# Performance work log

Measured on AMD Instinct MI355X. Metric: run time of the kernel, lower is better.

The kernel has to match this reference:

```python
import jax, jax.numpy as jnp
import numpy as np

NUM_HEADS = 12
EPS = 1e-5


def setup_inputs() -> dict:
    key = jax.random.key(0)
    k0, k1, k2 = jax.random.split(key, 3)
    B, C, D = 2, 768, 14  # batch, hidden_size, img_size//16
    x = jax.random.normal(k0, (B, C, D, D, D), dtype=jnp.float32)
    norm_w = jnp.ones((C,), dtype=jnp.float32)
    norm_b = jnp.zeros((C,), dtype=jnp.float32)
    qkv_w = jax.random.normal(k1, (3 * C, C), dtype=jnp.float32) * 0.02
    out_w = jax.random.normal(k2, (C, C), dtype=jnp.float32) * 0.02
    out_b = jnp.zeros((C,), dtype=jnp.float32)
    return {"x": x, "norm_w": norm_w, "norm_b": norm_b,
            "qkv_w": qkv_w, "out_w": out_w, "out_b": out_b}


def reference(x, norm_w, norm_b, qkv_w, out_w, out_b):
    B, C, D, H, W = x.shape
    nh = NUM_HEADS
    dh = C // nh
    scale = dh ** -0.5

    # b c d h w -> b (d h w) c
    t = jnp.transpose(x, (0, 2, 3, 4, 1)).reshape(B, D * H * W, C)
    N = t.shape[1]

    # LayerNorm over channel dim
    mu = jnp.mean(t, axis=-1, keepdims=True)
    var = jnp.mean(jnp.square(t - mu), axis=-1, keepdims=True)
    tn = (t - mu) / jnp.sqrt(var + EPS) * norm_w + norm_b

    # qkv projection (no bias), split as (3, heads, dim_head)
    qkv = tn @ qkv_w.T                       # [B, N, 3C]
    qkv = qkv.reshape(B, N, 3, nh, dh)
    qkv = jnp.transpose(qkv, (2, 0, 3, 1, 4))  # [3, B, nh, N, dh]
    q, k, v = qkv[0], qkv[1], qkv[2]

    att = jax.nn.softmax(jnp.einsum('blxn,blyn->blxy', q, k) * scale, axis=-1)
    out = jnp.einsum('blxy,blyn->blxn', att, v)  # [B, nh, N, dh]

    out = jnp.transpose(out, (0, 2, 1, 3)).reshape(B, N, C)
    out = out @ out_w.T + out_b

    out = out.reshape(B, D, H, W, C)
    out = jnp.transpose(out, (0, 4, 1, 2, 3))  # b d h w c -> b c d h w
    return out + x
```

## Files before the change

kernel.cpp:

```cpp
#include <hip/hip_runtime.h>

typedef unsigned short u16;
typedef unsigned int u32;

#define SPA 2744
#define CH  768
#define NH  12
#define DH  64
#define BB  2
#define TC  2304
#define MTOT (BB*SPA)
#define LNB 343
#define CVTB 2304

typedef __bf16 bf16x8_t __attribute__((ext_vector_type(8)));
typedef __bf16 bf16x4_t __attribute__((ext_vector_type(4)));
typedef short  s16x4    __attribute__((ext_vector_type(4)));
typedef float  f32x4_t  __attribute__((ext_vector_type(4)));

static __device__ __forceinline__ u16 f2bf(float f) {
    union { float f; u32 u; } v; v.f = f;
    u32 u = v.u;
    u += 0x7fffu + ((u >> 16) & 1u);
    return (u16)(u >> 16);
}

static __device__ __forceinline__ void gld16(const u16* g, u16* l) {
    __builtin_amdgcn_global_load_lds(
        (const __attribute__((address_space(1))) u32*)(size_t)g,
        (__attribute__((address_space(3))) u32*)(u32)(size_t)l, 16, 0, 0);
}

__global__ __launch_bounds__(256) void cvtln_kernel(const float* __restrict__ qkv_w,
                                                    u16* __restrict__ qkvw_bf, int n4a,
                                                    const float* __restrict__ out_w,
                                                    u16* __restrict__ outw_bf,
                                                    const float* __restrict__ x,
                                                    const float* __restrict__ w,
                                                    const float* __restrict__ bta,
                                                    u16* __restrict__ tn) {
    int tid = threadIdx.x;
    if (blockIdx.x >= LNB) {
        int i = (blockIdx.x - LNB) * 256 + tid;
        const float* src; u16* dst; int idx;
        if (i < n4a) { src = qkv_w; dst = qkvw_bf; idx = i; }
        else { src = out_w; dst = outw_bf; idx = i - n4a; }
        float4 f = ((const float4*)src)[idx];
        uint2 o;
        o.x = (u32)f2bf(f.x) | ((u32)f2bf(f.y) << 16);
        o.y = (u32)f2bf(f.z) | ((u32)f2bf(f.w) << 16);
        ((uint2*)dst)[idx] = o;
        return;
    }
    int bid = blockIdx.x;
    __shared__ f32x4_t redS[4][4];
    __shared__ f32x4_t redQ[4][4];
    __shared__ u16 T[64][22];
    int grp = tid & 3, chl = tid >> 2;
    int wvi = tid >> 6, lane = tid & 63;
    int tok0 = bid * 16 + grp * 4;
    int b = tok0 / SPA, n = tok0 - b * SPA;
    const float* base = x + (size_t)b * CH * SPA + n;

    f32x4_t s4 = {0.f, 0.f, 0.f, 0.f}, q4 = {0.f, 0.f, 0.f, 0.f};
    for (int c0 = 0; c0 < CH; c0 += 64) {
        float4 v = *(const float4*)(base + (size_t)(c0 + chl) * SPA);
        s4[0] += v.x; s4[1] += v.y; s4[2] += v.z; s4[3] += v.w;
        q4[0] += v.x * v.x; q4[1] += v.y * v.y; q4[2] += v.z * v.z; q4[3] += v.w * v.w;
    }
#pragma unroll
    for (int m = 4; m <= 32; m <<= 1)
#pragma unroll
        for (int e = 0; e < 4; e++) {
            s4[e] += __shfl_xor(s4[e], m);
            q4[e] += __shfl_xor(q4[e], m);
        }
    if (lane < 4) { redS[wvi][lane] = s4; redQ[wvi][lane] = q4; }
    __syncthreads();
    f32x4_t st = redS[0][grp], qt = redQ[0][grp];
#pragma unroll
    for (int wv2 = 1; wv2 < 4; wv2++) {
        f32x4_t a = redS[wv2][grp], c = redQ[wv2][grp];
#pragma unroll
        for (int e = 0; e < 4; e++) { st[e] += a[e]; qt[e] += c[e]; }
    }
    f32x4_t mean4, rstd4;
#pragma unroll
    for (int e = 0; e < 4; e++) {
        mean4[e] = st[e] * (1.0f / CH);
        rstd4[e] = rsqrtf(qt[e] * (1.0f / CH) - mean4[e] * mean4[e] + 1e-5f);
    }

    int tokl = tid >> 4, qq = tid & 15;
    int g2 = bid * 16 + tokl;
    for (int c0 = 0; c0 < CH; c0 += 64) {
        __syncthreads();
        {
            int cc = c0 + chl;
            float4 v = *(const float4*)(base + (size_t)cc * SPA);
            float ws = w[cc], bs = bta[cc];
            union { u16 h4[4]; uint2 u; } pk;
            pk.h4[0] = f2bf((v.x - mean4[0]) * rstd4[0] * ws + bs);
            pk.h4[1] = f2bf((v.y - mean4[1]) * rstd4[1] * ws + bs);
            pk.h4[2] = f2bf((v.z - mean4[2]) * rstd4[2] * ws + bs);
            pk.h4[3] = f2bf((v.w - mean4[3]) * rstd4[3] * ws + bs);
            *(uint2*)(&T[chl][grp * 4]) = pk.u;
        }
        __syncthreads();
        union { u16 h[4]; uint2 u; } pk;
#pragma unroll
        for (int e = 0; e < 4; e++) pk.h[e] = T[qq * 4 + e][tokl];
        *(uint2*)(tn + (size_t)g2 * CH + c0 + qq * 4) = pk.u;
    }
}

__global__ __launch_bounds__(256, 3) void gemm_qkv(const u16* __restrict__ A,
                                                   const u16* __restrict__ Bw,
                                                   u16* __restrict__ out0,
                                                   u16* __restrict__ out1,
                                                   u16* __restrict__ out2) {
    const int M = MTOT, K = CH;
    __shared__ __align__(16) u16 As[128 * 32];
    __shared__ __align__(16) u16 Bs[128 * 32];
    int tid = threadIdx.x;
    int m0 = blockIdx.y * 128;
    int n0 = blockIdx.x * 128;
    int wv = tid >> 6, lane = tid & 63;
    int wm = (wv >> 1) * 64, wn = (wv & 1) * 64;
    int quad = lane >> 4, l16 = lane & 15;

    f32x4_t zero = {0.f, 0.f, 0.f, 0.f};
    f32x4_t acc[4][4];
#pragma unroll
    for (int i = 0; i < 4; i++)
#pragma unroll
        for (int j = 0; j < 4; j++) acc[i][j] = zero;

    int rl = lane >> 2, pos = lane & 3;
    int sw = (l16 >> 1) & 3;
    for (int k0 = 0; k0 < K; k0 += 32) {
        __syncthreads();
#pragma unroll
        for (int p = 0; p < 2; p++) {
            int rbase = p * 64 + wv * 16;
            int row = rbase + rl;
            int gch = pos ^ ((row >> 1) & 3);
            int gm = m0 + row; if (gm >= M) gm = M - 1;
            gld16(A + (size_t)gm * K + k0 + gch * 8, As + rbase * 32);
            gld16(Bw + (size_t)(n0 + row) * K + k0 + gch * 8, Bs + rbase * 32);
        }
        __syncthreads();
        bf16x8_t af[4], bfr[4];
#pragma unroll
        for (int i = 0; i < 4; i++)
            af[i] = *(const bf16x8_t*)(As + (wm + i * 16 + l16) * 32 + ((quad ^ sw) * 8));
#pragma unroll
        for (int j = 0; j < 4; j++)
            bfr[j] = *(const bf16x8_t*)(Bs + (wn + j * 16 + l16) * 32 + ((quad ^ sw) * 8));
#pragma unroll
        for (int i = 0; i < 4; i++)
#pragma unroll
            for (int j = 0; j < 4; j++)
                acc[i][j] = __builtin_amdgcn_mfma_f32_16x16x32_bf16(af[i], bfr[j], acc[i][j], 0, 0, 0);
    }

    int which = n0 / CH;
    int rb = n0 - which * CH;
    u16* base = (which == 0) ? out0 : ((which == 1) ? out1 : out2);
    float qs = (which == 0) ? 0.18033688011112042f : 1.0f;
#pragma unroll
    for (int i = 0; i < 4; i++)
#pragma unroll
        for (int r = 0; r < 4; r++) {
            int gm = m0 + wm + i * 16 + quad * 4 + r;
            if (gm < M) {
                int b = gm / SPA, n = gm - b * SPA;
#pragma unroll
                for (int j = 0; j < 4; j++) {
                    int rem = rb + wn + j * 16 + l16;
                    int h = rem >> 6, d = rem & 63;
                    base[((size_t)(b * NH + h) * SPA + n) * DH + d] = f2bf(acc[i][j][r] * qs);
                }
            }
        }
}

__global__ __launch_bounds__(256, 4) void gemm_out(const u16* __restrict__ A,
                                                   const u16* __restrict__ Bw,
                                                   const float* __restrict__ xres,
                                                   const float* __restrict__ ob,
                                                   float* __restrict__ fout) {
    const int M = MTOT, K = CH;
    __shared__ __align__(16) u16 As[128 * 32];
    __shared__ __align__(16) u16 Bs[64 * 32];
    int tid = threadIdx.x;
    int m0 = blockIdx.y * 128;
    int n0 = blockIdx.x * 64;
    int wv = tid >> 6, lane = tid & 63;
    int wm = (wv >> 1) * 64, wn = (wv & 1) * 32;
    int quad = lane >> 4, l16 = lane & 15;

    f32x4_t zero = {0.f, 0.f, 0.f, 0.f};
    f32x4_t acc[4][2];
#pragma unroll
    for (int i = 0; i < 4; i++)
#pragma unroll
        for (int j = 0; j < 2; j++) acc[i][j] = zero;

    int rl = lane >> 2, pos = lane & 3;
    int sw = (l16 >> 1) & 3;
    for (int k0 = 0; k0 < K; k0 += 32) {
        __syncthreads();
#pragma unroll
        for (int p = 0; p < 2; p++) {
            int rbase = p * 64 + wv * 16;
            int row = rbase + rl;
            int gch = pos ^ ((row >> 1) & 3);
            int gm = m0 + row; if (gm >= M) gm = M - 1;
            gld16(A + (size_t)gm * K + k0 + gch * 8, As + rbase * 32);
        }
        {
            int row = wv * 16 + rl;
            int gch = pos ^ ((row >> 1) & 3);
            gld16(Bw + (size_t)(n0 + row) * K + k0 + gch * 8, Bs + (wv * 16) * 32);
        }
        __syncthreads();
        bf16x8_t af[4], bfr[2];
#pragma unroll
        for (int i = 0; i < 4; i++)
            af[i] = *(const bf16x8_t*)(As + (wm + i * 16 + l16) * 32 + ((quad ^ sw) * 8));
#pragma unroll
        for (int j = 0; j < 2; j++)
            bfr[j] = *(const bf16x8_t*)(Bs + (wn + j * 16 + l16) * 32 + ((quad ^ sw) * 8));
#pragma unroll
        for (int i = 0; i < 4; i++)
#pragma unroll
            for (int j = 0; j < 2; j++)
                acc[i][j] = __builtin_amdgcn_mfma_f32_16x16x32_bf16(af[i], bfr[j], acc[i][j], 0, 0, 0);
    }

#pragma unroll
    for (int i = 0; i < 4; i++) {
        int gm0 = m0 + wm + i * 16 + quad * 4;
        if (gm0 < M) {
            int b = gm0 / SPA;
            int n = gm0 - b * SPA;
#pragma unroll
            for (int j = 0; j < 2; j++) {
                int gn = n0 + wn + j * 16 + l16;
                size_t xo = ((size_t)(b * CH + gn)) * SPA + n;
                float4 xv = *(const float4*)(xres + xo);
                float bias = ob[gn];
                float4 rr;
                rr.x = xv.x + bias + acc[i][j][0];
                rr.y = xv.y + bias + acc[i][j][1];
                rr.z = xv.z + bias + acc[i][j][2];
                rr.w = xv.w + bias + acc[i][j][3];
                *(float4*)(fout + xo) = rr;
            }
        }
    }
}

__global__ __launch_bounds__(256) void vtrans_kernel(const u16* __restrict__ v,
                                                     u16* __restrict__ vt) {
    __shared__ __align__(16) u16 T[64 * 72];
    int bh = blockIdx.y;
    int n0 = blockIdx.x * 64;
    int tid = threadIdx.x;
#pragma unroll
    for (int h = 0; h < 2; h++) {
        int chunk = tid + h * 256;
        int r = chunk >> 3, cs = chunk & 7;
        int n = n0 + r;
        int4 val = make_int4(0, 0, 0, 0);
        if (n < SPA) val = *(const int4*)(v + ((size_t)bh * SPA + n) * DH + cs * 8);
        *(int4*)(T + r * 72 + cs * 8) = val;
    }
    __syncthreads();
#pragma unroll
    for (int h = 0; h < 2; h++) {
        int chunk = tid + h * 256;
        int d = chunk >> 3, cs = chunk & 7;
        int nb = n0 + cs * 8;
        if (nb < SPA) {
            union { u16 s[8]; int4 v4; } tmp;
#pragma unroll
            for (int e = 0; e < 8; e++) tmp.s[e] = T[(cs * 8 + e) * 72 + d];
            *(int4*)(vt + ((size_t)bh * DH + d) * SPA + nb) = tmp.v4;
        }
    }
}

__global__ __launch_bounds__(256, 3) void attn_kernel(const u16* __restrict__ q,
                                                      const u16* __restrict__ k,
                                                      const u16* __restrict__ vt,
                                                      u16* __restrict__ out) {
    __shared__ __align__(16) u16 Kbuf[2][96 * 64];
    __shared__ __align__(16) u16 Vbuf[2][64 * 108];
    int g = blockIdx.x;
    int xcd = g & 7, slot = g >> 3;
    int bh = xcd * 3 + slot % 3;
    int qg = slot / 3;
    int b = bh / NH, h = bh - b * NH;
    int tid = threadIdx.x;
    int wv = tid >> 6, lane = tid & 63;
    int quad = lane >> 4, l16 = lane & 15;
    int qhalf = wv & 1, khalf = wv >> 1;
    int koff = khalf * 48;
    int q0w = qg * 64 + qhalf * 32;

    const u16* qgp = q + (size_t)bh * SPA * DH;
    const u16* kg = k + (size_t)bh * SPA * DH;
    const u16* vg = vt + (size_t)bh * DH * SPA;

    bf16x8_t bq[2][2];
    int qglob[2];
#pragma unroll
    for (int qf = 0; qf < 2; qf++) {
        int qq = q0w + qf * 16 + l16;
        qglob[qf] = qq;
        int qld = (qq < SPA) ? qq : (SPA - 1);
#pragma unroll
        for (int ks = 0; ks < 2; ks++)
            bq[qf][ks] = *(const bf16x8_t*)(qgp + (size_t)qld * DH + ks * 32 + quad * 8);
    }

    f32x4_t zero = {0.f, 0.f, 0.f, 0.f};
    f32x4_t o[2][4];
#pragma unroll
    for (int qf = 0; qf < 2; qf++)
#pragma unroll
        for (int i = 0; i < 4; i++) o[qf][i] = zero;
    f32x4_t lacc[2];
    lacc[0] = zero; lacc[1] = zero;
    s16x4 ones;
    ones[0] = ones[1] = ones[2] = ones[3] = (short)0x3F80;

    int rl8 = lane >> 3, pos8 = lane & 7;
    int sw8 = l16 & 7;
    int vd = tid >> 2, vc = (tid & 3) * 24;

#pragma unroll
    for (int p = 0; p < 3; p++) {
        int rbase = p * 32 + wv * 8;
        int row = rbase + rl8;
        int gch = pos8 ^ (row & 7);
        gld16(kg + (size_t)row * DH + gch * 8, Kbuf[0] + rbase * 64);
    }
#pragma unroll
    for (int s2 = 0; s2 < 3; s2++)
        *(int4*)(Vbuf[0] + vd * 108 + vc + s2 * 8) =
            *(const int4*)(vg + (size_t)vd * SPA + vc + s2 * 8);

    for (int si = 0; si < 29; si++) {
        __syncthreads();
        int cur = si & 1, nxt = cur ^ 1;
        int kv0 = si * 96;
        bool hn = (si < 28);
        int4 vp0, vp1, vp2;
        if (hn) {
            int kb = kv0 + 96;
#pragma unroll
            for (int p = 0; p < 3; p++) {
                int rbase = p * 32 + wv * 8;
                int row = rbase + rl8;
                int gch = pos8 ^ (row & 7);
                int kr = kb + row; if (kr >= SPA) kr = SPA - 1;
                gld16(kg + (size_t)kr * DH + gch * 8, Kbuf[nxt] + rbase * 64);
            }
            int c0 = kb + vc;
            int a0 = c0;      if (a0 > SPA - 8) a0 = SPA - 8;
            int a1 = c0 + 8;  if (a1 > SPA - 8) a1 = SPA - 8;
            int a2 = c0 + 16; if (a2 > SPA - 8) a2 = SPA - 8;
            vp0 = *(const int4*)(vg + (size_t)vd * SPA + a0);
            vp1 = *(const int4*)(vg + (size_t)vd * SPA + a1);
            vp2 = *(const int4*)(vg + (size_t)vd * SPA + a2);
        }

        s16x4 bp[2][3];
#pragma unroll
        for (int i = 0; i < 3; i++) {
            const u16* krow = Kbuf[cur] + (koff + i * 16 + l16) * 64;
            bf16x8_t ak0 = *(const bf16x8_t*)(krow + ((quad ^ sw8) * 8));
            bf16x8_t ak1 = *(const bf16x8_t*)(krow + (((4 + quad) ^ sw8) * 8));
            f32x4_t s0 = __builtin_amdgcn_mfma_f32_16x16x32_bf16(ak0, bq[0][0], zero, 0, 0, 0);
            s0 = __builtin_amdgcn_mfma_f32_16x16x32_bf16(ak1, bq[0][1], s0, 0, 0, 0);
            f32x4_t s1 = __builtin_amdgcn_mfma_f32_16x16x32_bf16(ak0, bq[1][0], zero, 0, 0, 0);
            s1 = __builtin_amdgcn_mfma_f32_16x16x32_bf16(ak1, bq[1][1], s1, 0, 0, 0);
            bf16x4_t p0, p1;
            if (si != 28) {
#pragma unroll
                for (int r = 0; r < 4; r++) {
                    p0[r] = (__bf16)__builtin_amdgcn_exp2f(s0[r]);
                    p1[r] = (__bf16)__builtin_amdgcn_exp2f(s1[r]);
                }
            } else {
#pragma unroll
                for (int r = 0; r < 4; r++) {
                    float e0 = __builtin_amdgcn_exp2f(s0[r]);
                    float e1 = __builtin_amdgcn_exp2f(s1[r]);
                    bool bad = (kv0 + koff + i * 16 + quad * 4 + r) >= SPA;
                    p0[r] = (__bf16)(bad ? 0.f : e0);
                    p1[r] = (__bf16)(bad ? 0.f : e1);
                }
            }
            union { bf16x4_t b; s16x4 s; } u0, u1;
            u0.b = p0; u1.b = p1;
            bp[0][i] = u0.s; bp[1][i] = u1.s;
        }

        if (hn) {
            *(int4*)(Vbuf[nxt] + vd * 108 + vc)      = vp0;
            *(int4*)(Vbuf[nxt] + vd * 108 + vc + 8)  = vp1;
            *(int4*)(Vbuf[nxt] + vd * 108 + vc + 16) = vp2;
        }

#pragma unroll
        for (int c = 0; c < 3; c++) {
            lacc[0] = __builtin_amdgcn_mfma_f32_16x16x16bf16_1k(ones, bp[0][c], lacc[0], 0, 0, 0);
            lacc[1] = __builtin_amdgcn_mfma_f32_16x16x16bf16_1k(ones, bp[1][c], lacc[1], 0, 0, 0);
#pragma unroll
            for (int i = 0; i < 4; i++) {
                s16x4 av = *(const s16x4*)(Vbuf[cur] + (i * 16 + l16) * 108 + koff + c * 16 + quad * 4);
                o[0][i] = __builtin_amdgcn_mfma_f32_16x16x16bf16_1k(av, bp[0][c], o[0][i], 0, 0, 0);
                o[1][i] = __builtin_amdgcn_mfma_f32_16x16x16bf16_1k(av, bp[1][c], o[1][i], 0, 0, 0);
            }
        }
    }

    __syncthreads();
    float* lsh = (float*)Kbuf;
    if (wv >= 2) {
        int base = ((wv - 2) * 64 + lane) * 36;
#pragma unroll
        for (int qf = 0; qf < 2; qf++)
#pragma unroll
            for (int i = 0; i < 4; i++)
                *(f32x4_t*)(lsh + base + qf * 16 + i * 4) = o[qf][i];
        lsh[base + 32] = lacc[0][0];
        lsh[base + 33] = lacc[1][0];
    }
    __syncthreads();
    if (wv < 2) {
        int base = (wv * 64 + lane) * 36;
#pragma unroll
        for (int qf = 0; qf < 2; qf++)
#pragma unroll
            for (int i = 0; i < 4; i++) {
                f32x4_t t = *(const f32x4_t*)(lsh + base + qf * 16 + i * 4);
#pragma unroll
                for (int r = 0; r < 4; r++) o[qf][i][r] += t[r];
            }
        float lsum[2];
        lsum[0] = lacc[0][0] + lsh[base + 32];
        lsum[1] = lacc[1][0] + lsh[base + 33];
#pragma unroll
        for (int qf = 0; qf < 2; qf++) {
            int qq = qglob[qf];
            if (qq < SPA) {
                float inv = 1.0f / lsum[qf];
                u16* op = out + ((size_t)(b * SPA + qq)) * CH + h * DH;
#pragma unroll
                for (int i = 0; i < 4; i++) {
                    bf16x4_t ov;
#pragma unroll
                    for (int r = 0; r < 4; r++) ov[r] = (__bf16)(o[qf][i][r] * inv);
                    *(bf16x4_t*)(op + i * 16 + quad * 4) = ov;
                }
            }
        }
    }
}

extern "C" void kernel_launch(void* const* d_in, const int* in_sizes, int n_in,
                              void* d_out, int out_size, void* d_ws, size_t ws_size,
                              hipStream_t stream) {
    const float* x      = (const float*)d_in[0];
    const float* norm_w = (const float*)d_in[1];
    const float* norm_b = (const float*)d_in[2];
    const float* qkv_w  = (const float*)d_in[3];
    const float* out_w  = (const float*)d_in[4];
    const float* out_b  = (const float*)d_in[5];
    float* out = (float*)d_out;

    char* ws = (char*)d_ws;
    size_t off = 0;
    auto alloc = [&](size_t bytes) -> void* {
        void* p = ws + off;
        off += (bytes + 255) & ~(size_t)255;
        return p;
    };
    u16* tn      = (u16*)alloc((size_t)MTOT * CH * 2);
    u16* qkvw_bf = (u16*)alloc((size_t)TC * CH * 2);
    u16* outw_bf = (u16*)alloc((size_t)CH * CH * 2);
    u16* qb      = (u16*)alloc((size_t)BB * NH * SPA * DH * 2);
    u16* kb      = (u16*)alloc((size_t)BB * NH * SPA * DH * 2);
    u16* vb      = (u16*)alloc((size_t)BB * NH * SPA * DH * 2);
    u16* vtb     = (u16*)alloc((size_t)BB * NH * SPA * DH * 2);
    u16* ao      = (u16*)alloc((size_t)MTOT * CH * 2);

    int n4a = TC * CH / 4;
    cvtln_kernel<<<LNB + CVTB, 256, 0, stream>>>(
        qkv_w, qkvw_bf, n4a, out_w, outw_bf, x, norm_w, norm_b, tn);
    gemm_qkv<<<dim3(TC / 128, (MTOT + 127) / 128), 256, 0, stream>>>(
        tn, qkvw_bf, qb, kb, vb);
    vtrans_kernel<<<dim3((SPA + 63) / 64, BB * NH), 256, 0, stream>>>(vb, vtb);
    attn_kernel<<<1032, 256, 0, stream>>>(qb, kb, vtb, ao);
    gemm_out<<<dim3(CH / 64, (MTOT + 127) / 128), 256, 0, stream>>>(
        ao, outw_bf, x, out_b, out);
}
```

Before: 234.2 us.

## Fuse V transpose into QKV GEMM epilogue and drop vtrans kernel

The QKV GEMM blocks that produce V now transpose their 128x128 tile through per-wave shared-memory buffers and write V directly in the [bh, d, n] layout the attention kernel consumes. This removes the separate vtrans kernel launch, the intermediate V buffer, and one full read and write of V in global memory. In exchange, gemm_qkv gains about 36KB of static LDS, which may limit occupancy at the 3-blocks-per-CU launch bound. The V tiles are also stored as 16-byte column chunks with strided rows instead of the previous coalesced layout.

```diff
diff --git a/kernel.cpp b/kernel.cpp
--- a/kernel.cpp
+++ b/kernel.cpp
@@ -118,10 +118,11 @@
                                                    const u16* __restrict__ Bw,
                                                    u16* __restrict__ out0,
                                                    u16* __restrict__ out1,
-                                                   u16* __restrict__ out2) {
+                                                   u16* __restrict__ vtb) {
     const int M = MTOT, K = CH;
     __shared__ __align__(16) u16 As[128 * 32];
     __shared__ __align__(16) u16 Bs[128 * 32];
+    __shared__ __align__(16) u16 Tv[4][64 * 72];
     int tid = threadIdx.x;
     int m0 = blockIdx.y * 128;
     int n0 = blockIdx.x * 128;
@@ -166,7 +167,35 @@
 
     int which = n0 / CH;
     int rb = n0 - which * CH;
-    u16* base = (which == 0) ? out0 : ((which == 1) ? out1 : out2);
+
+    if (which == 2) {
+        u16* Twv = &Tv[wv][0];
+#pragma unroll
+        for (int i = 0; i < 4; i++)
+#pragma unroll
+            for (int j = 0; j < 4; j++) {
+                union { u16 h4[4]; uint2 u; } pk;
+#pragma unroll
+                for (int r = 0; r < 4; r++) pk.h4[r] = f2bf(acc[i][j][r]);
+                *(uint2*)(&Twv[(j * 16 + l16) * 72 + i * 16 + quad * 4]) = pk.u;
+            }
+        int rd = lane >> 3, tc8 = (lane & 7) * 8;
+#pragma unroll
+        for (int rr = 0; rr < 8; rr++) {
+            int row = rr * 8 + rd;
+            int rem = rb + wn + row;
+            int hh = rem >> 6, dd = rem & 63;
+            int t0 = m0 + wm + tc8;
+            if (t0 < MTOT) {
+                int b2 = t0 / SPA, n2 = t0 - b2 * SPA;
+                *(int4*)(vtb + ((size_t)(b2 * NH + hh) * DH + dd) * SPA + n2) =
+                    *(const int4*)(&Twv[row * 72 + tc8]);
+            }
+        }
+        return;
+    }
+
+    u16* base = (which == 0) ? out0 : out1;
     float qs = (which == 0) ? 0.18033688011112042f : 1.0f;
 #pragma unroll
     for (int i = 0; i < 4; i++)
@@ -258,36 +287,6 @@
                 rr.w = xv.w + bias + acc[i][j][3];
                 *(float4*)(fout + xo) = rr;
             }
-        }
-    }
-}
-
-__global__ __launch_bounds__(256) void vtrans_kernel(const u16* __restrict__ v,
-                                                     u16* __restrict__ vt) {
-    __shared__ __align__(16) u16 T[64 * 72];
-    int bh = blockIdx.y;
-    int n0 = blockIdx.x * 64;
-    int tid = threadIdx.x;
-#pragma unroll
-    for (int h = 0; h < 2; h++) {
-        int chunk = tid + h * 256;
-        int r = chunk >> 3, cs = chunk & 7;
-        int n = n0 + r;
-        int4 val = make_int4(0, 0, 0, 0);
-        if (n < SPA) val = *(const int4*)(v + ((size_t)bh * SPA + n) * DH + cs * 8);
-        *(int4*)(T + r * 72 + cs * 8) = val;
-    }
-    __syncthreads();
-#pragma unroll
-    for (int h = 0; h < 2; h++) {
-        int chunk = tid + h * 256;
-        int d = chunk >> 3, cs = chunk & 7;
-        int nb = n0 + cs * 8;
-        if (nb < SPA) {
-            union { u16 s[8]; int4 v4; } tmp;
-#pragma unroll
-            for (int e = 0; e < 8; e++) tmp.s[e] = T[(cs * 8 + e) * 72 + d];
-            *(int4*)(vt + ((size_t)bh * DH + d) * SPA + nb) = tmp.v4;
         }
     }
 }
@@ -496,7 +495,6 @@
     u16* outw_bf = (u16*)alloc((size_t)CH * CH * 2);
     u16* qb      = (u16*)alloc((size_t)BB * NH * SPA * DH * 2);
     u16* kb      = (u16*)alloc((size_t)BB * NH * SPA * DH * 2);
-    u16* vb      = (u16*)alloc((size_t)BB * NH * SPA * DH * 2);
     u16* vtb     = (u16*)alloc((size_t)BB * NH * SPA * DH * 2);
     u16* ao      = (u16*)alloc((size_t)MTOT * CH * 2);
 
@@ -504,8 +502,7 @@
     cvtln_kernel<<<LNB + CVTB, 256, 0, stream>>>(
         qkv_w, qkvw_bf, n4a, out_w, outw_bf, x, norm_w, norm_b, tn);
     gemm_qkv<<<dim3(TC / 128, (MTOT + 127) / 128), 256, 0, stream>>>(
-        tn, qkvw_bf, qb, kb, vb);
-    vtrans_kernel<<<dim3((SPA + 63) / 64, BB * NH), 256, 0, stream>>>(vb, vtb);
+        tn, qkvw_bf, qb, kb, vtb);
     attn_kernel<<<1032, 256, 0, stream>>>(qb, kb, vtb, ao);
     gemm_out<<<dim3(CH / 64, (MTOT + 127) / 128), 256, 0, stream>>>(
         ao, outw_bf, x, out_b, out);
```

Measured after the change: 234.7 us. Within noise of the previous version (+0.2%).
